# Optimization experiments

Hardware: AMD Instinct MI355X
Metric: run time of the kernel (lower is better)

The kernel has to match this reference:

```python
import jax, jax.numpy as jnp
import numpy as np

N = 50000      # nodes
E = 800000     # edges (avg degree 16)
G = 128        # graphs in batch
IN = 128       # in_channels
H = 128        # hidden_dim
C = 10         # num_classes


def setup_inputs() -> dict:
    key = jax.random.key(0)
    ks = jax.random.split(key, 8)
    x = jax.random.normal(ks[0], (N, IN), dtype=jnp.float32)
    edge_index = jax.random.randint(ks[1], (2, E), 0, N)
    edge_attr = jax.random.uniform(ks[2], (E,), dtype=jnp.float32)
    batch = jnp.sort(jax.random.randint(ks[3], (N,), 0, G))
    def glorot(k, fan_in, fan_out):
        return jax.random.normal(k, (fan_in, fan_out), dtype=jnp.float32) / np.float32(np.sqrt(fan_in))
    return {
        "x": x,
        "edge_index": edge_index,
        "edge_attr": edge_attr,
        "batch": batch,
        "W1": glorot(ks[4], IN, H), "b1": jnp.zeros((H,), jnp.float32),
        "W2": glorot(ks[5], H, H), "b2": jnp.zeros((H,), jnp.float32),
        "W3": glorot(ks[6], H, C), "b3": jnp.zeros((C,), jnp.float32),
    }


def gcn_conv(x, src, dst, ew, W, b, n):
    # symmetric GCN normalization (self-loops already appended, weight 1)
    deg = jax.ops.segment_sum(ew, dst, num_segments=n)            # [N]
    dinv = jnp.where(deg > 0, jax.lax.rsqrt(deg), 0.0)
    norm = dinv[src] * ew * dinv[dst]                             # [E+N]
    h = x @ W                                                     # [N, out]
    agg = jax.ops.segment_sum(h[src] * norm[:, None], dst, num_segments=n)
    return agg + b


def reference(x, edge_index, edge_attr, batch, W1, b1, W2, b2, W3, b3):
    n = x.shape[0]
    loop = jnp.arange(n)
    src = jnp.concatenate([edge_index[0], loop])
    dst = jnp.concatenate([edge_index[1], loop])
    ew = jnp.concatenate([edge_attr, jnp.ones((n,), edge_attr.dtype)])
    h = jax.nn.relu(gcn_conv(x, src, dst, ew, W1, b1, n))   # dropout is identity in eval
    h = jax.nn.relu(gcn_conv(h, src, dst, ew, W2, b2, n))
    h = gcn_conv(h, src, dst, ew, W3, b3, n)                 # [N, C]
    # global mean pool over graphs
    sums = jax.ops.segment_sum(h, batch, num_segments=G)     # [G, C]
    cnt = jax.ops.segment_sum(jnp.ones((n,), h.dtype), batch, num_segments=G)
    pooled = sums / jnp.maximum(cnt, 1.0)[:, None]
    return jax.nn.log_softmax(pooled, axis=1)
```

## Files before the change

### kernel.cpp

```cpp
#include <hip/hip_runtime.h>

#define NN 50000
#define NE 800000
#define NG 128
#define DIM 128
#define CO 10
#define CAP 64
#define NB 2048

typedef unsigned long long ull;
typedef unsigned short ushort;
typedef unsigned int uint;
typedef __attribute__((ext_vector_type(8))) short short8;
typedef __attribute__((ext_vector_type(4))) float floatx4;

static __device__ __forceinline__ ushort f2bf(float f) {
    uint u = __float_as_uint(f);
    uint r = (u + 0x7FFF + ((u >> 16) & 1)) >> 16;
    return (ushort)r;
}
#define EWS (1.0f / 65535.0f)

__global__ void k_ell(const int* __restrict__ src, const int* __restrict__ dst,
                      const float* __restrict__ ew, int* __restrict__ cnt,
                      uint* __restrict__ ell) {
    int e = blockIdx.x * blockDim.x + threadIdx.x;
    if (e >= NE) return;
    int d = dst[e], s = src[e];
    int slot = atomicAdd(&cnt[d], 1);
    if (slot < CAP) {
        uint w16 = (uint)__float2uint_rn(ew[e] * 65535.0f);
        ell[(size_t)d * CAP + slot] = (w16 << 16) | (uint)s;
    }
}

__global__ __launch_bounds__(256) void k_deg(const int* __restrict__ cnt,
                                             const uint* __restrict__ ell,
                                             float* __restrict__ dinv) {
    int node = blockIdx.x * 4 + (threadIdx.x >> 6);
    int lane = threadIdx.x & 63;
    if (node >= NN) return;
    int n = cnt[node];
    float w = 0.0f;
    if (lane < n) w = (float)(ell[(size_t)node * CAP + lane] >> 16) * EWS;
#pragma unroll
    for (int off = 32; off; off >>= 1) w += __shfl_down(w, off);
    if (lane == 0) dinv[node] = rsqrtf(1.0f + w);
}

__global__ void k_prepw(const float* __restrict__ W, ushort* __restrict__ Wt) {
    int i = blockIdx.x * blockDim.x + threadIdx.x;
    int k = i >> 7, n = i & 127;
    Wt[n * 128 + k] = f2bf(W[i]);
}

__global__ __launch_bounds__(256) void k_gemm_mfma(const void* __restrict__ Ain, int abf,
                                                   const ushort* __restrict__ Wt,
                                                   const float* __restrict__ dinv,
                                                   ushort* __restrict__ C, int M) {
    int wave = threadIdx.x >> 6;
    int lane = threadIdx.x & 63;
    int quad = lane >> 4;
    int mcol = lane & 15;
    int r0 = blockIdx.x * 64 + wave * 16;
    int arow = r0 + mcol;
    if (arow >= M) arow = M - 1;
    floatx4 acc[8];
#pragma unroll
    for (int t = 0; t < 8; t++) acc[t] = (floatx4){0.0f, 0.0f, 0.0f, 0.0f};

    const ushort* Ab = (const ushort*)Ain;
    const float*  Af = (const float*)Ain;
#pragma unroll
    for (int kk = 0; kk < 4; kk++) {
        int koff = kk * 32 + quad * 8;
        short8 a;
        if (abf) {
            a = *(const short8*)&Ab[(size_t)arow * 128 + koff];
        } else {
            const float* ap = &Af[(size_t)arow * 128 + koff];
            float4 x0 = *(const float4*)ap;
            float4 x1 = *(const float4*)(ap + 4);
            union { short8 v; ushort u[8]; } ua;
            ua.u[0] = f2bf(x0.x); ua.u[1] = f2bf(x0.y); ua.u[2] = f2bf(x0.z); ua.u[3] = f2bf(x0.w);
            ua.u[4] = f2bf(x1.x); ua.u[5] = f2bf(x1.y); ua.u[6] = f2bf(x1.z); ua.u[7] = f2bf(x1.w);
            a = ua.v;
        }
#pragma unroll
        for (int t = 0; t < 8; t++) {
            short8 b = *(const short8*)&Wt[(size_t)(t * 16 + mcol) * 128 + koff];
            acc[t] = __builtin_amdgcn_mfma_f32_16x16x32_bf16(a, b, acc[t], 0, 0, 0);
        }
    }
#pragma unroll
    for (int reg = 0; reg < 4; reg++) {
        int row = r0 + quad * 4 + reg;
        if (row < M) {
            float di = dinv[row];
            ushort* cp = &C[(size_t)row * 128];
#pragma unroll
            for (int t = 0; t < 8; t++) cp[t * 16 + mcol] = f2bf(di * acc[t][reg]);
        }
    }
}

__global__ __launch_bounds__(256) void k_gemm10(const ushort* __restrict__ A,
                                                const float* __restrict__ W3,
                                                const float* __restrict__ dinv,
                                                float* __restrict__ C3, int M) {
    __shared__ float Ws[1280];
    int tid = threadIdx.x;
    for (int i = tid; i < 1280; i += 256) Ws[i] = W3[i];
    __syncthreads();
    int col = tid & 15;
    int rloc = tid >> 4;
    int row = blockIdx.x * 16 + rloc;
    if (row >= M || col >= 10) return;
    const ushort* a = &A[(size_t)row * 128];
    float acc = 0.0f;
#pragma unroll
    for (int k = 0; k < 128; k += 4) {
        ushort4 av = *(const ushort4*)&a[k];
        acc += __uint_as_float((uint)av.x << 16) * Ws[(k + 0) * 10 + col];
        acc += __uint_as_float((uint)av.y << 16) * Ws[(k + 1) * 10 + col];
        acc += __uint_as_float((uint)av.z << 16) * Ws[(k + 2) * 10 + col];
        acc += __uint_as_float((uint)av.w << 16) * Ws[(k + 3) * 10 + col];
    }
    C3[(size_t)row * 10 + col] = dinv[row] * acc;
}

__global__ __launch_bounds__(256) void k_gather128(const int* __restrict__ cnt,
                                                   const uint* __restrict__ ell,
                                                   const float* __restrict__ dinv,
                                                   const ushort* __restrict__ h,
                                                   const float* __restrict__ b,
                                                   ushort* __restrict__ outp) {
    int node = blockIdx.x * 4 + (threadIdx.x >> 6);
    int lane = threadIdx.x & 63;
    if (node >= NN) return;
    int n = cnt[node];
    uint hp = *(const uint*)&h[(size_t)node * 128 + lane * 2];
    float ax = __uint_as_float(hp << 16);
    float ay = __uint_as_float(hp & 0xffff0000u);
    uint rec = ell[(size_t)node * CAP + lane];
    int ce = (int)(rec & 0xffffu);
    float we = (float)(rec >> 16) * EWS;
    int j = 0;
    for (; j + 3 < n; j += 4) {
        int s0 = __shfl(ce, j + 0), s1 = __shfl(ce, j + 1);
        int s2 = __shfl(ce, j + 2), s3 = __shfl(ce, j + 3);
        float w0 = __shfl(we, j + 0), w1 = __shfl(we, j + 1);
        float w2 = __shfl(we, j + 2), w3 = __shfl(we, j + 3);
        uint p0 = *(const uint*)&h[(size_t)s0 * 128 + lane * 2];
        uint p1 = *(const uint*)&h[(size_t)s1 * 128 + lane * 2];
        uint p2 = *(const uint*)&h[(size_t)s2 * 128 + lane * 2];
        uint p3 = *(const uint*)&h[(size_t)s3 * 128 + lane * 2];
        ax += w0 * __uint_as_float(p0 << 16) + w1 * __uint_as_float(p1 << 16)
            + w2 * __uint_as_float(p2 << 16) + w3 * __uint_as_float(p3 << 16);
        ay += w0 * __uint_as_float(p0 & 0xffff0000u) + w1 * __uint_as_float(p1 & 0xffff0000u)
            + w2 * __uint_as_float(p2 & 0xffff0000u) + w3 * __uint_as_float(p3 & 0xffff0000u);
    }
    for (; j < n; j++) {
        int s0 = __shfl(ce, j);
        float w0 = __shfl(we, j);
        uint p0 = *(const uint*)&h[(size_t)s0 * 128 + lane * 2];
        ax += w0 * __uint_as_float(p0 << 16);
        ay += w0 * __uint_as_float(p0 & 0xffff0000u);
    }
    float di = dinv[node];
    ax = fmaxf(di * ax + b[lane * 2 + 0], 0.0f);
    ay = fmaxf(di * ay + b[lane * 2 + 1], 0.0f);
    uint o = ((uint)f2bf(ay) << 16) | (uint)f2bf(ax);
    *(uint*)&outp[(size_t)node * 128 + lane * 2] = o;
}

__global__ __launch_bounds__(256) void k_pool_node(const int* __restrict__ cnt,
                                                   const uint* __restrict__ ell,
                                                   const float* __restrict__ dinv,
                                                   const float* __restrict__ z,
                                                   const int* __restrict__ batch,
                                                   float* __restrict__ partial) {
    __shared__ float ls[NG * CO + NG];
    for (int i = threadIdx.x; i < NG * CO + NG; i += 256) ls[i] = 0.0f;
    __syncthreads();
    int lane = threadIdx.x & 63;
    int gwave = blockIdx.x * 4 + (threadIdx.x >> 6);
    for (int node = gwave; node < NN; node += NB * 4) {
        int n = cnt[node];
        float w = 0.0f; int s = 0;
        if (lane < n) {
            uint rec = ell[(size_t)node * CAP + lane];
            s = (int)(rec & 0xffffu);
            w = (float)(rec >> 16) * EWS;
        } else if (lane == n) {
            s = node;
            w = 1.0f;
        }
        const float* zp = &z[(size_t)s * 10];
        float v[10];
#pragma unroll
        for (int f = 0; f < 10; f++) v[f] = w * zp[f];
#pragma unroll
        for (int off = 32; off; off >>= 1) {
#pragma unroll
            for (int f = 0; f < 10; f++) v[f] += __shfl_down(v[f], off);
        }
        if (lane == 0) {
            int g = batch[node];
            float di = dinv[node];
            float* lp = &ls[g * 10];
#pragma unroll
            for (int f = 0; f < 10; f++) atomicAdd(&lp[f], di * v[f]);
            atomicAdd(&ls[NG * CO + g], 1.0f);
        }
    }
    __syncthreads();
    float* pb = &partial[(size_t)blockIdx.x * (NG * CO + NG)];
    for (int i = threadIdx.x; i < NG * CO + NG; i += 256) pb[i] = ls[i];
}

__global__ __launch_bounds__(256) void k_pool_final(const float* __restrict__ partial,
                                                    const float* __restrict__ b3,
                                                    float* __restrict__ out) {
    __shared__ float red[4][11];
    int g = blockIdx.x;
    int t = threadIdx.x;
    int lane = t & 63, wv = t >> 6;
    float v[10]; float c = 0.0f;
#pragma unroll
    for (int f = 0; f < 10; f++) v[f] = 0.0f;
    for (int b = t; b < NB; b += 256) {
        const float* pb = &partial[(size_t)b * (NG * CO + NG)];
#pragma unroll
        for (int f = 0; f < 10; f++) v[f] += pb[g * 10 + f];
        c += pb[NG * CO + g];
    }
#pragma unroll
    for (int off = 32; off; off >>= 1) {
#pragma unroll
        for (int f = 0; f < 10; f++) v[f] += __shfl_down(v[f], off);
        c += __shfl_down(c, off);
    }
    if (lane == 0) {
#pragma unroll
        for (int f = 0; f < 10; f++) red[wv][f] = v[f];
        red[wv][10] = c;
    }
    __syncthreads();
    if (t == 0) {
        float p[10], m = -1e30f;
        float cc = red[0][10] + red[1][10] + red[2][10] + red[3][10];
        cc = fmaxf(cc, 1.0f);
#pragma unroll
        for (int f = 0; f < 10; f++) {
            p[f] = (red[0][f] + red[1][f] + red[2][f] + red[3][f]) / cc + b3[f];
            m = fmaxf(m, p[f]);
        }
        float ssum = 0.0f;
#pragma unroll
        for (int f = 0; f < 10; f++) ssum += __expf(p[f] - m);
        float lse = m + __logf(ssum);
#pragma unroll
        for (int f = 0; f < 10; f++) out[g * 10 + f] = p[f] - lse;
    }
}

extern "C" void kernel_launch(void* const* d_in, const int* in_sizes, int n_in,
                              void* d_out, int out_size, void* d_ws, size_t ws_size,
                              hipStream_t stream) {
    const float* x     = (const float*)d_in[0];
    const int*   ei    = (const int*)d_in[1];
    const float* ea    = (const float*)d_in[2];
    const int*   batch = (const int*)d_in[3];
    const float* W1    = (const float*)d_in[4];
    const float* b1    = (const float*)d_in[5];
    const float* W2    = (const float*)d_in[6];
    const float* b2    = (const float*)d_in[7];
    const float* W3    = (const float*)d_in[8];
    const float* b3    = (const float*)d_in[9];
    float* out = (float*)d_out;
    float* ws  = (float*)d_ws;

    const int* esrc = ei;
    const int* edst = ei + NE;

    ushort* hb      = (ushort*)ws;
    ushort* gb      = (ushort*)(ws + 3200000);
    float*  z       = ws + 6400000;
    float*  dinv    = ws + 6900000;
    int*    cnt     = (int*)(ws + 6950000);
    uint*   ell     = (uint*)(ws + 7000000);
    ushort* wt1     = (ushort*)(ws + 10200000);
    ushort* wt2     = (ushort*)(ws + 10210000);
    float*  partial = (float*)hb;

    hipMemsetAsync(cnt, 0, NN * sizeof(int), stream);
    k_ell<<<(NE + 255) / 256, 256, 0, stream>>>(esrc, edst, ea, cnt, ell);
    k_prepw<<<64, 256, 0, stream>>>(W1, wt1);
    k_prepw<<<64, 256, 0, stream>>>(W2, wt2);
    k_deg<<<(NN + 3) / 4, 256, 0, stream>>>(cnt, ell, dinv);

    k_gemm_mfma<<<(NN + 63) / 64, 256, 0, stream>>>(x, 0, wt1, dinv, hb, NN);
    k_gather128<<<(NN + 3) / 4, 256, 0, stream>>>(cnt, ell, dinv, hb, b1, gb);

    k_gemm_mfma<<<(NN + 63) / 64, 256, 0, stream>>>(gb, 1, wt2, dinv, hb, NN);
    k_gather128<<<(NN + 3) / 4, 256, 0, stream>>>(cnt, ell, dinv, hb, b2, gb);

    k_gemm10<<<(NN + 15) / 16, 256, 0, stream>>>(gb, W3, dinv, z, NN);
    k_pool_node<<<NB, 256, 0, stream>>>(cnt, ell, dinv, z, batch, partial);
    k_pool_final<<<NG, 256, 0, stream>>>(partial, b3, out);
}
```

Before: 312.5 us.

## Overlap ELL build with first GEMM and merge prep kernels

```diff
diff --git a/kernel.cpp b/kernel.cpp
--- a/kernel.cpp
+++ b/kernel.cpp
@@ -7,6 +7,8 @@
 #define CO 10
 #define CAP 64
 #define NB 2048
+#define ELLB 3125
+#define GEMB 782
 
 typedef unsigned long long ull;
 typedef unsigned short ushort;
@@ -21,54 +23,35 @@
 }
 #define EWS (1.0f / 65535.0f)
 
-__global__ void k_ell(const int* __restrict__ src, const int* __restrict__ dst,
-                      const float* __restrict__ ew, int* __restrict__ cnt,
-                      uint* __restrict__ ell) {
-    int e = blockIdx.x * blockDim.x + threadIdx.x;
-    if (e >= NE) return;
-    int d = dst[e], s = src[e];
-    int slot = atomicAdd(&cnt[d], 1);
-    if (slot < CAP) {
-        uint w16 = (uint)__float2uint_rn(ew[e] * 65535.0f);
-        ell[(size_t)d * CAP + slot] = (w16 << 16) | (uint)s;
-    }
-}
-
-__global__ __launch_bounds__(256) void k_deg(const int* __restrict__ cnt,
-                                             const uint* __restrict__ ell,
-                                             float* __restrict__ dinv) {
-    int node = blockIdx.x * 4 + (threadIdx.x >> 6);
-    int lane = threadIdx.x & 63;
-    if (node >= NN) return;
-    int n = cnt[node];
-    float w = 0.0f;
-    if (lane < n) w = (float)(ell[(size_t)node * CAP + lane] >> 16) * EWS;
-#pragma unroll
-    for (int off = 32; off; off >>= 1) w += __shfl_down(w, off);
-    if (lane == 0) dinv[node] = rsqrtf(1.0f + w);
-}
-
-__global__ void k_prepw(const float* __restrict__ W, ushort* __restrict__ Wt) {
-    int i = blockIdx.x * blockDim.x + threadIdx.x;
-    int k = i >> 7, n = i & 127;
-    Wt[n * 128 + k] = f2bf(W[i]);
-}
-
-__global__ __launch_bounds__(256) void k_gemm_mfma(const void* __restrict__ Ain, int abf,
-                                                   const ushort* __restrict__ Wt,
-                                                   const float* __restrict__ dinv,
-                                                   ushort* __restrict__ C, int M) {
-    int wave = threadIdx.x >> 6;
-    int lane = threadIdx.x & 63;
+__global__ void k_prep(const float* __restrict__ W1, const float* __restrict__ W2,
+                       ushort* __restrict__ wt1, ushort* __restrict__ wt2,
+                       int* __restrict__ cnt) {
+    int bid = blockIdx.x;
+    int tid = threadIdx.x;
+    if (bid < 64) {
+        int i = bid * 256 + tid;
+        int k = i >> 7, n = i & 127;
+        wt1[n * 128 + k] = f2bf(W1[i]);
+    } else if (bid < 128) {
+        int i = (bid - 64) * 256 + tid;
+        int k = i >> 7, n = i & 127;
+        wt2[n * 128 + k] = f2bf(W2[i]);
+    } else {
+        int i = (bid - 128) * 256 + tid;
+        if (i < NN) cnt[i] = 0;
+    }
+}
+
+static __device__ __forceinline__ void gemm_tile(const void* Ain, int abf,
+                                                 const ushort* Wt, const float* dscale,
+                                                 ushort* C, int M, int r0, int lane) {
     int quad = lane >> 4;
     int mcol = lane & 15;
-    int r0 = blockIdx.x * 64 + wave * 16;
     int arow = r0 + mcol;
     if (arow >= M) arow = M - 1;
     floatx4 acc[8];
 #pragma unroll
     for (int t = 0; t < 8; t++) acc[t] = (floatx4){0.0f, 0.0f, 0.0f, 0.0f};
-
     const ushort* Ab = (const ushort*)Ain;
     const float*  Af = (const float*)Ain;
 #pragma unroll
@@ -96,12 +79,60 @@
     for (int reg = 0; reg < 4; reg++) {
         int row = r0 + quad * 4 + reg;
         if (row < M) {
-            float di = dinv[row];
+            float di = dscale ? dscale[row] : 1.0f;
             ushort* cp = &C[(size_t)row * 128];
 #pragma unroll
             for (int t = 0; t < 8; t++) cp[t * 16 + mcol] = f2bf(di * acc[t][reg]);
         }
     }
+}
+
+__global__ __launch_bounds__(256) void k_fused(const int* __restrict__ src,
+                                               const int* __restrict__ dst,
+                                               const float* __restrict__ ew,
+                                               int* __restrict__ cnt,
+                                               uint* __restrict__ ell,
+                                               const float* __restrict__ x,
+                                               const ushort* __restrict__ wt1,
+                                               ushort* __restrict__ hraw) {
+    int bid = blockIdx.x;
+    if (bid < ELLB) {
+        int e = bid * 256 + threadIdx.x;
+        int d = dst[e], s = src[e];
+        int slot = atomicAdd(&cnt[d], 1);
+        if (slot < CAP) {
+            uint w16 = (uint)__float2uint_rn(ew[e] * 65535.0f);
+            ell[(size_t)d * CAP + slot] = (w16 << 16) | (uint)s;
+        }
+    } else {
+        int gb = bid - ELLB;
+        int wave = threadIdx.x >> 6;
+        int lane = threadIdx.x & 63;
+        gemm_tile(x, 0, wt1, nullptr, hraw, NN, gb * 64 + wave * 16, lane);
+    }
+}
+
+__global__ __launch_bounds__(256) void k_deg(const int* __restrict__ cnt,
+                                             const uint* __restrict__ ell,
+                                             float* __restrict__ dinv) {
+    int node = blockIdx.x * 4 + (threadIdx.x >> 6);
+    int lane = threadIdx.x & 63;
+    if (node >= NN) return;
+    int n = cnt[node];
+    float w = 0.0f;
+    if (lane < n) w = (float)(ell[(size_t)node * CAP + lane] >> 16) * EWS;
+#pragma unroll
+    for (int off = 32; off; off >>= 1) w += __shfl_down(w, off);
+    if (lane == 0) dinv[node] = rsqrtf(1.0f + w);
+}
+
+__global__ __launch_bounds__(256) void k_gemm_mfma(const ushort* __restrict__ A,
+                                                   const ushort* __restrict__ Wt,
+                                                   const float* __restrict__ dinv,
+                                                   ushort* __restrict__ C, int M) {
+    int wave = threadIdx.x >> 6;
+    int lane = threadIdx.x & 63;
+    gemm_tile(A, 1, Wt, dinv, C, M, blockIdx.x * 64 + wave * 16, lane);
 }
 
 __global__ __launch_bounds__(256) void k_gemm10(const ushort* __restrict__ A,
@@ -134,17 +165,21 @@
                                                    const float* __restrict__ dinv,
                                                    const ushort* __restrict__ h,
                                                    const float* __restrict__ b,
-                                                   ushort* __restrict__ outp) {
+                                                   ushort* __restrict__ outp,
+                                                   int scaled) {
     int node = blockIdx.x * 4 + (threadIdx.x >> 6);
     int lane = threadIdx.x & 63;
     if (node >= NN) return;
     int n = cnt[node];
-    uint hp = *(const uint*)&h[(size_t)node * 128 + lane * 2];
-    float ax = __uint_as_float(hp << 16);
-    float ay = __uint_as_float(hp & 0xffff0000u);
+    float di = dinv[node];
     uint rec = ell[(size_t)node * CAP + lane];
     int ce = (int)(rec & 0xffffu);
     float we = (float)(rec >> 16) * EWS;
+    if (!scaled) we *= dinv[ce];
+    uint hp = *(const uint*)&h[(size_t)node * 128 + lane * 2];
+    float selfw = scaled ? 1.0f : di;
+    float ax = selfw * __uint_as_float(hp << 16);
+    float ay = selfw * __uint_as_float(hp & 0xffff0000u);
     int j = 0;
     for (; j + 3 < n; j += 4) {
         int s0 = __shfl(ce, j + 0), s1 = __shfl(ce, j + 1);
@@ -167,7 +202,6 @@
         ax += w0 * __uint_as_float(p0 << 16);
         ay += w0 * __uint_as_float(p0 & 0xffff0000u);
     }
-    float di = dinv[node];
     ax = fmaxf(di * ax + b[lane * 2 + 0], 0.0f);
     ay = fmaxf(di * ay + b[lane * 2 + 1], 0.0f);
     uint o = ((uint)f2bf(ay) << 16) | (uint)f2bf(ax);
@@ -294,17 +328,16 @@
     ushort* wt2     = (ushort*)(ws + 10210000);
     float*  partial = (float*)hb;
 
-    hipMemsetAsync(cnt, 0, NN * sizeof(int), stream);
-    k_ell<<<(NE + 255) / 256, 256, 0, stream>>>(esrc, edst, ea, cnt, ell);
-    k_prepw<<<64, 256, 0, stream>>>(W1, wt1);
-    k_prepw<<<64, 256, 0, stream>>>(W2, wt2);
+    k_prep<<<128 + 196, 256, 0, stream>>>(W1, W2, wt1, wt2, cnt);
+
+    k_fused<<<ELLB + GEMB, 256, 0, stream>>>(esrc, edst, ea, cnt, ell, x, wt1, hb);
+
     k_deg<<<(NN + 3) / 4, 256, 0, stream>>>(cnt, ell, dinv);
 
-    k_gemm_mfma<<<(NN + 63) / 64, 256, 0, stream>>>(x, 0, wt1, dinv, hb, NN);
-    k_gather128<<<(NN + 3) / 4, 256, 0, stream>>>(cnt, ell, dinv, hb, b1, gb);
-
-    k_gemm_mfma<<<(NN + 63) / 64, 256, 0, stream>>>(gb, 1, wt2, dinv, hb, NN);
-    k_gather128<<<(NN + 3) / 4, 256, 0, stream>>>(cnt, ell, dinv, hb, b2, gb);
+    k_gather128<<<(NN + 3) / 4, 256, 0, stream>>>(cnt, ell, dinv, hb, b1, gb, 0);
+
+    k_gemm_mfma<<<GEMB, 256, 0, stream>>>(gb, wt2, dinv, hb, NN);
+    k_gather128<<<(NN + 3) / 4, 256, 0, stream>>>(cnt, ell, dinv, hb, b2, gb, 1);
 
     k_gemm10<<<(NN + 15) / 16, 256, 0, stream>>>(gb, W3, dinv, z, NN);
     k_pool_node<<<NB, 256, 0, stream>>>(cnt, ell, dinv, z, batch, partial);
```

Result: no change. 315.7 us (+1.0%).

## Fuse GCN pipeline kernels: prep, degree into GEMM, W3 into gather, single-pass pool

Applied to the files above, without the earlier changes.

```diff
diff --git a/kernel.cpp b/kernel.cpp
--- a/kernel.cpp
+++ b/kernel.cpp
@@ -6,9 +6,9 @@
 #define DIM 128
 #define CO 10
 #define CAP 64
-#define NB 2048
-
-typedef unsigned long long ull;
+#define NPB 2048
+#define GEMB 782
+
 typedef unsigned short ushort;
 typedef unsigned int uint;
 typedef __attribute__((ext_vector_type(8))) short short8;
@@ -20,6 +20,25 @@
     return (ushort)r;
 }
 #define EWS (1.0f / 65535.0f)
+
+__global__ void k_prep(const float* __restrict__ W1, const float* __restrict__ W2,
+                       ushort* __restrict__ wt1, ushort* __restrict__ wt2,
+                       int* __restrict__ cnt, float* __restrict__ sums,
+                       int* __restrict__ done) {
+    int i = blockIdx.x * 256 + threadIdx.x;
+    if (i < 16384) {
+        wt1[(i & 127) * 128 + (i >> 7)] = f2bf(W1[i]);
+    } else if (i < 32768) {
+        int j = i - 16384;
+        wt2[(j & 127) * 128 + (j >> 7)] = f2bf(W2[j]);
+    } else if (i < 32768 + NN) {
+        cnt[i - 32768] = 0;
+    } else if (i < 32768 + NN + NG * CO + NG) {
+        sums[i - 32768 - NN] = 0.0f;
+    } else if (i == 32768 + NN + NG * CO + NG) {
+        *done = 0;
+    }
+}
 
 __global__ void k_ell(const int* __restrict__ src, const int* __restrict__ dst,
                       const float* __restrict__ ew, int* __restrict__ cnt,
@@ -34,41 +53,17 @@
     }
 }
 
-__global__ __launch_bounds__(256) void k_deg(const int* __restrict__ cnt,
-                                             const uint* __restrict__ ell,
-                                             float* __restrict__ dinv) {
-    int node = blockIdx.x * 4 + (threadIdx.x >> 6);
-    int lane = threadIdx.x & 63;
-    if (node >= NN) return;
-    int n = cnt[node];
-    float w = 0.0f;
-    if (lane < n) w = (float)(ell[(size_t)node * CAP + lane] >> 16) * EWS;
-#pragma unroll
-    for (int off = 32; off; off >>= 1) w += __shfl_down(w, off);
-    if (lane == 0) dinv[node] = rsqrtf(1.0f + w);
-}
-
-__global__ void k_prepw(const float* __restrict__ W, ushort* __restrict__ Wt) {
-    int i = blockIdx.x * blockDim.x + threadIdx.x;
-    int k = i >> 7, n = i & 127;
-    Wt[n * 128 + k] = f2bf(W[i]);
-}
-
-__global__ __launch_bounds__(256) void k_gemm_mfma(const void* __restrict__ Ain, int abf,
-                                                   const ushort* __restrict__ Wt,
-                                                   const float* __restrict__ dinv,
-                                                   ushort* __restrict__ C, int M) {
-    int wave = threadIdx.x >> 6;
-    int lane = threadIdx.x & 63;
+static __device__ __forceinline__ void gemm_tile(const void* Ain, int abf,
+                                                 const ushort* Wt,
+                                                 const float* dglob, const float* dlds,
+                                                 ushort* C, int M, int r0, int lane) {
     int quad = lane >> 4;
     int mcol = lane & 15;
-    int r0 = blockIdx.x * 64 + wave * 16;
     int arow = r0 + mcol;
     if (arow >= M) arow = M - 1;
     floatx4 acc[8];
 #pragma unroll
     for (int t = 0; t < 8; t++) acc[t] = (floatx4){0.0f, 0.0f, 0.0f, 0.0f};
-
     const ushort* Ab = (const ushort*)Ain;
     const float*  Af = (const float*)Ain;
 #pragma unroll
@@ -96,7 +91,7 @@
     for (int reg = 0; reg < 4; reg++) {
         int row = r0 + quad * 4 + reg;
         if (row < M) {
-            float di = dinv[row];
+            float di = dglob ? dglob[row] : (dlds ? dlds[quad * 4 + reg] : 1.0f);
             ushort* cp = &C[(size_t)row * 128];
 #pragma unroll
             for (int t = 0; t < 8; t++) cp[t * 16 + mcol] = f2bf(di * acc[t][reg]);
@@ -104,47 +99,60 @@
     }
 }
 
-__global__ __launch_bounds__(256) void k_gemm10(const ushort* __restrict__ A,
-                                                const float* __restrict__ W3,
-                                                const float* __restrict__ dinv,
-                                                float* __restrict__ C3, int M) {
-    __shared__ float Ws[1280];
-    int tid = threadIdx.x;
-    for (int i = tid; i < 1280; i += 256) Ws[i] = W3[i];
-    __syncthreads();
-    int col = tid & 15;
-    int rloc = tid >> 4;
-    int row = blockIdx.x * 16 + rloc;
-    if (row >= M || col >= 10) return;
-    const ushort* a = &A[(size_t)row * 128];
-    float acc = 0.0f;
-#pragma unroll
-    for (int k = 0; k < 128; k += 4) {
-        ushort4 av = *(const ushort4*)&a[k];
-        acc += __uint_as_float((uint)av.x << 16) * Ws[(k + 0) * 10 + col];
-        acc += __uint_as_float((uint)av.y << 16) * Ws[(k + 1) * 10 + col];
-        acc += __uint_as_float((uint)av.z << 16) * Ws[(k + 2) * 10 + col];
-        acc += __uint_as_float((uint)av.w << 16) * Ws[(k + 3) * 10 + col];
-    }
-    C3[(size_t)row * 10 + col] = dinv[row] * acc;
-}
-
-__global__ __launch_bounds__(256) void k_gather128(const int* __restrict__ cnt,
-                                                   const uint* __restrict__ ell,
-                                                   const float* __restrict__ dinv,
-                                                   const ushort* __restrict__ h,
-                                                   const float* __restrict__ b,
-                                                   ushort* __restrict__ outp) {
+__global__ __launch_bounds__(256) void k_gemm1(const float* __restrict__ x,
+                                               const ushort* __restrict__ wt1,
+                                               const int* __restrict__ cnt,
+                                               const uint* __restrict__ ell,
+                                               float* __restrict__ dinv,
+                                               ushort* __restrict__ hb) {
+    __shared__ float sdinv[4][16];
+    int wv = threadIdx.x >> 6;
+    int lane = threadIdx.x & 63;
+    int r0 = blockIdx.x * 64 + wv * 16;
+#pragma unroll 4
+    for (int r = 0; r < 16; r++) {
+        int row = r0 + r;
+        if (row < NN) {
+            int n = cnt[row];
+            float w = (lane < n) ? (float)(ell[(size_t)row * CAP + lane] >> 16) * EWS : 0.0f;
+#pragma unroll
+            for (int off = 32; off; off >>= 1) w += __shfl_down(w, off);
+            if (lane == 0) {
+                float dv = rsqrtf(1.0f + w);
+                dinv[row] = dv;
+                sdinv[wv][r] = dv;
+            }
+        }
+    }
+    gemm_tile(x, 0, wt1, nullptr, &sdinv[wv][0], hb, NN, r0, lane);
+}
+
+__global__ __launch_bounds__(256) void k_gemm2(const ushort* __restrict__ A,
+                                               const ushort* __restrict__ wt2,
+                                               const float* __restrict__ dinv,
+                                               ushort* __restrict__ C) {
+    int wv = threadIdx.x >> 6;
+    int lane = threadIdx.x & 63;
+    gemm_tile(A, 1, wt2, dinv, nullptr, C, NN, blockIdx.x * 64 + wv * 16, lane);
+}
+
+__global__ __launch_bounds__(256) void k_gather1(const int* __restrict__ cnt,
+                                                 const uint* __restrict__ ell,
+                                                 const float* __restrict__ dinv,
+                                                 const ushort* __restrict__ h,
+                                                 const float* __restrict__ b,
+                                                 ushort* __restrict__ outp) {
     int node = blockIdx.x * 4 + (threadIdx.x >> 6);
     int lane = threadIdx.x & 63;
     if (node >= NN) return;
     int n = cnt[node];
+    float di = dinv[node];
+    uint rec = ell[(size_t)node * CAP + lane];
+    int ce = (int)(rec & 0xffffu);
+    float we = (float)(rec >> 16) * EWS;
     uint hp = *(const uint*)&h[(size_t)node * 128 + lane * 2];
     float ax = __uint_as_float(hp << 16);
     float ay = __uint_as_float(hp & 0xffff0000u);
-    uint rec = ell[(size_t)node * CAP + lane];
-    int ce = (int)(rec & 0xffffu);
-    float we = (float)(rec >> 16) * EWS;
     int j = 0;
     for (; j + 3 < n; j += 4) {
         int s0 = __shfl(ce, j + 0), s1 = __shfl(ce, j + 1);
@@ -167,25 +175,93 @@
         ax += w0 * __uint_as_float(p0 << 16);
         ay += w0 * __uint_as_float(p0 & 0xffff0000u);
     }
-    float di = dinv[node];
     ax = fmaxf(di * ax + b[lane * 2 + 0], 0.0f);
     ay = fmaxf(di * ay + b[lane * 2 + 1], 0.0f);
     uint o = ((uint)f2bf(ay) << 16) | (uint)f2bf(ax);
     *(uint*)&outp[(size_t)node * 128 + lane * 2] = o;
 }
 
-__global__ __launch_bounds__(256) void k_pool_node(const int* __restrict__ cnt,
-                                                   const uint* __restrict__ ell,
-                                                   const float* __restrict__ dinv,
-                                                   const float* __restrict__ z,
-                                                   const int* __restrict__ batch,
-                                                   float* __restrict__ partial) {
-    __shared__ float ls[NG * CO + NG];
-    for (int i = threadIdx.x; i < NG * CO + NG; i += 256) ls[i] = 0.0f;
-    __syncthreads();
+__global__ __launch_bounds__(256) void k_gather2z(const int* __restrict__ cnt,
+                                                  const uint* __restrict__ ell,
+                                                  const float* __restrict__ dinv,
+                                                  const ushort* __restrict__ h,
+                                                  const float* __restrict__ b,
+                                                  const float* __restrict__ W3,
+                                                  float* __restrict__ z) {
     int lane = threadIdx.x & 63;
     int gwave = blockIdx.x * 4 + (threadIdx.x >> 6);
-    for (int node = gwave; node < NN; node += NB * 4) {
+    float w3a[10], w3b[10];
+    const float* wrow = &W3[lane * 20];
+#pragma unroll
+    for (int f = 0; f < 10; f++) { w3a[f] = wrow[f]; w3b[f] = wrow[10 + f]; }
+    float bx = b[lane * 2 + 0], by = b[lane * 2 + 1];
+
+    for (int node = gwave; node < NN; node += 12500) {
+        int n = cnt[node];
+        float di = dinv[node];
+        uint rec = ell[(size_t)node * CAP + lane];
+        int ce = (int)(rec & 0xffffu);
+        float we = (float)(rec >> 16) * EWS;
+        uint hp = *(const uint*)&h[(size_t)node * 128 + lane * 2];
+        float ax = __uint_as_float(hp << 16);
+        float ay = __uint_as_float(hp & 0xffff0000u);
+        int j = 0;
+        for (; j + 3 < n; j += 4) {
+            int s0 = __shfl(ce, j + 0), s1 = __shfl(ce, j + 1);
+            int s2 = __shfl(ce, j + 2), s3 = __shfl(ce, j + 3);
+            float w0 = __shfl(we, j + 0), w1 = __shfl(we, j + 1);
+            float w2 = __shfl(we, j + 2), w3 = __shfl(we, j + 3);
+            uint p0 = *(const uint*)&h[(size_t)s0 * 128 + lane * 2];
+            uint p1 = *(const uint*)&h[(size_t)s1 * 128 + lane * 2];
+            uint p2 = *(const uint*)&h[(size_t)s2 * 128 + lane * 2];
+            uint p3 = *(const uint*)&h[(size_t)s3 * 128 + lane * 2];
+            ax += w0 * __uint_as_float(p0 << 16) + w1 * __uint_as_float(p1 << 16)
+                + w2 * __uint_as_float(p2 << 16) + w3 * __uint_as_float(p3 << 16);
+            ay += w0 * __uint_as_float(p0 & 0xffff0000u) + w1 * __uint_as_float(p1 & 0xffff0000u)
+                + w2 * __uint_as_float(p2 & 0xffff0000u) + w3 * __uint_as_float(p3 & 0xffff0000u);
+        }
+        for (; j < n; j++) {
+            int s0 = __shfl(ce, j);
+            float w0 = __shfl(we, j);
+            uint p0 = *(const uint*)&h[(size_t)s0 * 128 + lane * 2];
+            ax += w0 * __uint_as_float(p0 << 16);
+            ay += w0 * __uint_as_float(p0 & 0xffff0000u);
+        }
+        ax = fmaxf(di * ax + bx, 0.0f);
+        ay = fmaxf(di * ay + by, 0.0f);
+        float p[10];
+#pragma unroll
+        for (int f = 0; f < 10; f++) p[f] = ax * w3a[f] + ay * w3b[f];
+#pragma unroll
+        for (int off = 32; off; off >>= 1) {
+#pragma unroll
+            for (int f = 0; f < 10; f++) p[f] += __shfl_down(p[f], off);
+        }
+        if (lane == 0) {
+            float* zp = &z[(size_t)node * 10];
+#pragma unroll
+            for (int f = 0; f < 10; f++) zp[f] = di * p[f];
+        }
+    }
+}
+
+__global__ __launch_bounds__(256) void k_pool(const int* __restrict__ cnt,
+                                              const uint* __restrict__ ell,
+                                              const float* __restrict__ dinv,
+                                              const float* __restrict__ z,
+                                              const int* __restrict__ batch,
+                                              float* __restrict__ sums,
+                                              int* __restrict__ done,
+                                              const float* __restrict__ b3,
+                                              float* __restrict__ out) {
+    __shared__ float ls[NG * CO + NG];
+    __shared__ int last;
+    int tid = threadIdx.x;
+    for (int i = tid; i < NG * CO + NG; i += 256) ls[i] = 0.0f;
+    __syncthreads();
+    int lane = tid & 63;
+    int gwave = blockIdx.x * 4 + (tid >> 6);
+    for (int node = gwave; node < NN; node += NPB * 4) {
         int n = cnt[node];
         float w = 0.0f; int s = 0;
         if (lane < n) {
@@ -215,45 +291,24 @@
         }
     }
     __syncthreads();
-    float* pb = &partial[(size_t)blockIdx.x * (NG * CO + NG)];
-    for (int i = threadIdx.x; i < NG * CO + NG; i += 256) pb[i] = ls[i];
-}
-
-__global__ __launch_bounds__(256) void k_pool_final(const float* __restrict__ partial,
-                                                    const float* __restrict__ b3,
-                                                    float* __restrict__ out) {
-    __shared__ float red[4][11];
-    int g = blockIdx.x;
-    int t = threadIdx.x;
-    int lane = t & 63, wv = t >> 6;
-    float v[10]; float c = 0.0f;
-#pragma unroll
-    for (int f = 0; f < 10; f++) v[f] = 0.0f;
-    for (int b = t; b < NB; b += 256) {
-        const float* pb = &partial[(size_t)b * (NG * CO + NG)];
-#pragma unroll
-        for (int f = 0; f < 10; f++) v[f] += pb[g * 10 + f];
-        c += pb[NG * CO + g];
-    }
-#pragma unroll
-    for (int off = 32; off; off >>= 1) {
-#pragma unroll
-        for (int f = 0; f < 10; f++) v[f] += __shfl_down(v[f], off);
-        c += __shfl_down(c, off);
-    }
-    if (lane == 0) {
-#pragma unroll
-        for (int f = 0; f < 10; f++) red[wv][f] = v[f];
-        red[wv][10] = c;
-    }
+    for (int i = tid; i < NG * CO + NG; i += 256) {
+        float v = ls[i];
+        if (v != 0.0f) atomicAdd(&sums[i], v);
+    }
+    __threadfence();
+    if (tid == 0) last = (atomicAdd(done, 1) == NPB - 1);
     __syncthreads();
-    if (t == 0) {
+    if (last && tid < NG) {
+        int g = tid;
+        float cc = __hip_atomic_load(&sums[NG * CO + g], __ATOMIC_RELAXED,
+                                     __HIP_MEMORY_SCOPE_AGENT);
+        cc = fmaxf(cc, 1.0f);
         float p[10], m = -1e30f;
-        float cc = red[0][10] + red[1][10] + red[2][10] + red[3][10];
-        cc = fmaxf(cc, 1.0f);
 #pragma unroll
         for (int f = 0; f < 10; f++) {
-            p[f] = (red[0][f] + red[1][f] + red[2][f] + red[3][f]) / cc + b3[f];
+            float sv = __hip_atomic_load(&sums[g * 10 + f], __ATOMIC_RELAXED,
+                                         __HIP_MEMORY_SCOPE_AGENT);
+            p[f] = sv / cc + b3[f];
             m = fmaxf(m, p[f]);
         }
         float ssum = 0.0f;
@@ -284,29 +339,22 @@
     const int* esrc = ei;
     const int* edst = ei + NE;
 
-    ushort* hb      = (ushort*)ws;
-    ushort* gb      = (ushort*)(ws + 3200000);
-    float*  z       = ws + 6400000;
-    float*  dinv    = ws + 6900000;
-    int*    cnt     = (int*)(ws + 6950000);
-    uint*   ell     = (uint*)(ws + 7000000);
-    ushort* wt1     = (ushort*)(ws + 10200000);
-    ushort* wt2     = (ushort*)(ws + 10210000);
-    float*  partial = (float*)hb;
-
-    hipMemsetAsync(cnt, 0, NN * sizeof(int), stream);
+    ushort* hb   = (ushort*)ws;
+    ushort* gb   = (ushort*)(ws + 3200000);
+    float*  z    = ws + 6400000;
+    float*  dinv = ws + 6900000;
+    int*    cnt  = (int*)(ws + 6950000);
+    uint*   ell  = (uint*)(ws + 7000000);
+    ushort* wt1  = (ushort*)(ws + 10200000);
+    ushort* wt2  = (ushort*)(ws + 10210000);
+    float*  sums = ws + 10220000;
+    int*    done = (int*)(ws + 10221500);
+
+    k_prep<<<330, 256, 0, stream>>>(W1, W2, wt1, wt2, cnt, sums, done);
     k_ell<<<(NE + 255) / 256, 256, 0, stream>>>(esrc, edst, ea, cnt, ell);
-    k_prepw<<<64, 256, 0, stream>>>(W1, wt1);
-    k_prepw<<<64, 256, 0, stream>>>(W2, wt2);
-    k_deg<<<(NN + 3) / 4, 256, 0, stream>>>(cnt, ell, dinv);
-
-    k_gemm_mfma<<<(NN + 63) / 64, 256, 0, stream>>>(x, 0, wt1, dinv, hb, NN);
-    k_gather128<<<(NN + 3) / 4, 256, 0, stream>>>(cnt, ell, dinv, hb, b1, gb);
-
-    k_gemm_mfma<<<(NN + 63) / 64, 256, 0, stream>>>(gb, 1, wt2, dinv, hb, NN);
-    k_gather128<<<(NN + 3) / 4, 256, 0, stream>>>(cnt, ell, dinv, hb, b2, gb);
-
-    k_gemm10<<<(NN + 15) / 16, 256, 0, stream>>>(gb, W3, dinv, z, NN);
-    k_pool_node<<<NB, 256, 0, stream>>>(cnt, ell, dinv, z, batch, partial);
-    k_pool_final<<<NG, 256, 0, stream>>>(partial, b3, out);
-}
+    k_gemm1<<<GEMB, 256, 0, stream>>>(x, wt1, cnt, ell, dinv, hb);
+    k_gather1<<<(NN + 3) / 4, 256, 0, stream>>>(cnt, ell, dinv, hb, b1, gb);
+    k_gemm2<<<GEMB, 256, 0, stream>>>(gb, wt2, dinv, hb);
+    k_gather2z<<<3125, 256, 0, stream>>>(cnt, ell, dinv, hb, b2, W3, z);
+    k_pool<<<NPB, 256, 0, stream>>>(cnt, ell, dinv, z, batch, sums, done, b3, out);
+}
```

New measurement: 432.5 us. +38.4%, slower.
